# Performance work log

Hardware: AMD Instinct MI355X
Metric: run time of the kernel (lower is better)

The kernel has to match this reference:

```python
import jax, jax.numpy as jnp
import numpy as np

N, E, DIN, H0, H1, HEADS = 50000, 600000, 128, 64, 64, 4
NEG_SLOPE = 0.2
BN_EPS = 1e-5


def setup_inputs() -> dict:
    key = jax.random.key(0)
    ks = iter(jax.random.split(key, 40))
    def p(shape, s=0.05):
        return jax.random.normal(next(ks), shape, jnp.float32) * s
    inp = {}
    inp['x'] = jax.random.normal(next(ks), (N, DIN), jnp.float32)
    inp['edge_index'] = jax.random.randint(next(ks), (2, E), 0, N, dtype=jnp.int32)
    inp['gcn1_w'] = p((DIN, H0)); inp['gcn1_b'] = p((H0,))
    inp['gcn2_w'] = p((H0, H1)); inp['gcn2_b'] = p((H1,))
    inp['gat1_w'] = p((DIN, HEADS * H0))
    inp['gat1_asrc'] = p((HEADS, H0)); inp['gat1_adst'] = p((HEADS, H0))
    inp['gat1_b'] = p((HEADS * H0,))
    inp['gat2_w'] = p((HEADS * H0, H1))
    inp['gat2_asrc'] = p((1, H1)); inp['gat2_adst'] = p((1, H1))
    inp['gat2_b'] = p((H1,))
    inp['sage1_wl'] = p((DIN, H0)); inp['sage1_bl'] = p((H0,)); inp['sage1_wr'] = p((DIN, H0))
    inp['sage2_wl'] = p((H0, H1)); inp['sage2_bl'] = p((H1,)); inp['sage2_wr'] = p((H0, H1))
    inp['bn_gcn_g'] = jnp.ones((H1,), jnp.float32); inp['bn_gcn_b'] = jnp.zeros((H1,), jnp.float32)
    inp['bn_gat_g'] = jnp.ones((H1,), jnp.float32); inp['bn_gat_b'] = jnp.zeros((H1,), jnp.float32)
    inp['bn_sage_g'] = jnp.ones((H1,), jnp.float32); inp['bn_sage_b'] = jnp.zeros((H1,), jnp.float32)
    inp['fc1_w'] = p((3 * H1, H1)); inp['fc1_b'] = p((H1,))
    inp['fc2_w'] = p((H1, 2)); inp['fc2_b'] = p((2,))
    return inp


def _gcn(x, w, b, src, dst, n):
    h = x @ w
    loop = jnp.arange(n)
    s = jnp.concatenate([src, loop]); d = jnp.concatenate([dst, loop])
    deg = jax.ops.segment_sum(jnp.ones(d.shape, h.dtype), d, n)
    dinv = jax.lax.rsqrt(jnp.maximum(deg, 1.0))  # deg >= 1 due to self-loops
    norm = dinv[s] * dinv[d]
    out = jax.ops.segment_sum(h[s] * norm[:, None], d, n)
    return out + b


def _gat(x, w, asrc, adst, b, src, dst, n, heads, outc, concat):
    # GATConv with self-loops; per-destination softmax over incoming edges
    h = (x @ w).reshape(n, heads, outc)
    loop = jnp.arange(n)
    s = jnp.concatenate([src, loop]); d = jnp.concatenate([dst, loop])
    a_s = jnp.einsum('nhc,hc->nh', h, asrc)
    a_d = jnp.einsum('nhc,hc->nh', h, adst)
    e = a_s[s] + a_d[d]                           # [Etot, H]
    e = jnp.where(e > 0, e, NEG_SLOPE * e)        # leaky relu
    emax = jax.ops.segment_max(e, d, n)           # every node has a self-loop
    ex = jnp.exp(e - emax[d])
    denom = jax.ops.segment_sum(ex, d, n)
    alpha = ex / (denom[d] + 1e-16)               # [Etot, H]
    out = jax.ops.segment_sum(h[s] * alpha[:, :, None], d, n)  # [n, H, C]
    out = out.reshape(n, heads * outc) if concat else out.mean(axis=1)
    return out + b


def _sage(x, wl, bl, wr, src, dst, n):
    # SAGEConv (mean aggr): lin_l(mean_j x_j) + lin_r(x_i)
    deg = jax.ops.segment_sum(jnp.ones(src.shape, x.dtype), dst, n)
    agg = jax.ops.segment_sum(x[src], dst, n) / jnp.maximum(deg, 1.0)[:, None]
    return agg @ wl + bl + x @ wr


def _bn(x, g, b):
    m = x.mean(0)
    v = x.var(0)
    return (x - m) * jax.lax.rsqrt(v + BN_EPS) * g + b


def reference(x, edge_index, gcn1_w, gcn1_b, gcn2_w, gcn2_b,
              gat1_w, gat1_asrc, gat1_adst, gat1_b,
              gat2_w, gat2_asrc, gat2_adst, gat2_b,
              sage1_wl, sage1_bl, sage1_wr, sage2_wl, sage2_bl, sage2_wr,
              bn_gcn_g, bn_gcn_b, bn_gat_g, bn_gat_b, bn_sage_g, bn_sage_b,
              fc1_w, fc1_b, fc2_w, fc2_b):
    src, dst = edge_index[0], edge_index[1]
    n = x.shape[0]
    g = jax.nn.relu(_gcn(x, gcn1_w, gcn1_b, src, dst, n))
    g = _bn(jax.nn.relu(_gcn(g, gcn2_w, gcn2_b, src, dst, n)), bn_gcn_g, bn_gcn_b)
    a = jax.nn.elu(_gat(x, gat1_w, gat1_asrc, gat1_adst, gat1_b, src, dst, n, HEADS, H0, True))
    a = _bn(jax.nn.elu(_gat(a, gat2_w, gat2_asrc, gat2_adst, gat2_b, src, dst, n, 1, H1, False)), bn_gat_g, bn_gat_b)
    s = jax.nn.relu(_sage(x, sage1_wl, sage1_bl, sage1_wr, src, dst, n))
    s = _bn(jax.nn.relu(_sage(s, sage2_wl, sage2_bl, sage2_wr, src, dst, n)), bn_sage_g, bn_sage_b)
    out = jnp.concatenate([g, a, s], axis=-1)
    h = jax.nn.relu(out @ fc1_w + fc1_b)
    return h @ fc2_w + fc2_b
```

## Files before the change

kernel.cpp:

```cpp
#include <hip/hip_runtime.h>
#include <math.h>

#define NEG_SLOPE 0.2f
#define BN_EPS 1e-5f

typedef short short8 __attribute__((ext_vector_type(8)));
typedef float floatx16 __attribute__((ext_vector_type(16)));

__device__ __forceinline__ float d_leaky(float x){ return x > 0.f ? x : NEG_SLOPE * x; }
__device__ __forceinline__ float d_elu(float x){ return x > 0.f ? x : expm1f(x); }

__device__ __forceinline__ unsigned short f2bf_rne(float f){
  unsigned int u = __float_as_uint(f);
  unsigned int r = (u + 0x7fffu + ((u >> 16) & 1u)) >> 16;
  return (unsigned short)r;
}
__device__ __forceinline__ float bf2f(unsigned short h){ return __uint_as_float((unsigned int)h << 16); }
__device__ __forceinline__ float2 bf2x(unsigned int u){
  float2 r;
  r.x = __uint_as_float(u << 16);
  r.y = __uint_as_float(u & 0xffff0000u);
  return r;
}

__device__ __forceinline__ float wave_sum(float v){
  #pragma unroll
  for (int off = 32; off > 0; off >>= 1) v += __shfl_xor(v, off, 64);
  return v;
}
__device__ __forceinline__ int wave_scan_incl(int v, int lane){
  #pragma unroll
  for (int off = 1; off < 64; off <<= 1){
    int u = __shfl_up(v, off, 64);
    if (lane >= off) v += u;
  }
  return v;
}

__global__ void k_count(const int* __restrict__ dst, int* __restrict__ deg, int E){
  int e = blockIdx.x * blockDim.x + threadIdx.x;
  if (e < E) atomicAdd(&deg[dst[e]], 1);
}

__global__ __launch_bounds__(256) void k_scan_a(const int* __restrict__ deg, int* __restrict__ bsum, int n){
  int t = threadIdx.x;
  int base = blockIdx.x * 1024 + t * 4;
  int d0=0,d1=0,d2=0,d3=0;
  if (base + 3 < n){ int4 v = *(const int4*)(deg + base); d0=v.x; d1=v.y; d2=v.z; d3=v.w; }
  else {
    if (base   < n) d0 = deg[base];
    if (base+1 < n) d1 = deg[base+1];
    if (base+2 < n) d2 = deg[base+2];
    if (base+3 < n) d3 = deg[base+3];
  }
  int s = d0+d1+d2+d3;
  __shared__ int wsm[4];
  int lane = t & 63, w = t >> 6;
  int incl = wave_scan_incl(s, lane);
  if (lane == 63) wsm[w] = incl;
  __syncthreads();
  if (t == 0) bsum[blockIdx.x] = wsm[0]+wsm[1]+wsm[2]+wsm[3];
}

__global__ void k_scan_b(int* __restrict__ bsum, int* __restrict__ rowp, int nb, int n){
  int t = threadIdx.x;
  int v = (t < nb) ? bsum[t] : 0;
  int incl = wave_scan_incl(v, t);
  if (t < nb) bsum[t] = incl - v;
  if (t == 63) rowp[n] = incl;
}

__global__ __launch_bounds__(256) void k_scan_c(const int* __restrict__ deg, const int* __restrict__ bsum,
                                                int* __restrict__ rowp, float* __restrict__ dinv,
                                                float* __restrict__ sdinv, int n){
  int t = threadIdx.x;
  int base = blockIdx.x * 1024 + t * 4;
  int d0=0,d1=0,d2=0,d3=0;
  if (base + 3 < n){ int4 v = *(const int4*)(deg + base); d0=v.x; d1=v.y; d2=v.z; d3=v.w; }
  else {
    if (base   < n) d0 = deg[base];
    if (base+1 < n) d1 = deg[base+1];
    if (base+2 < n) d2 = deg[base+2];
    if (base+3 < n) d3 = deg[base+3];
  }
  int s = d0+d1+d2+d3;
  __shared__ int wsm[4];
  int lane = t & 63, w = t >> 6;
  int incl = wave_scan_incl(s, lane);
  if (lane == 63) wsm[w] = incl;
  __syncthreads();
  int woff = 0;
  #pragma unroll
  for (int j = 0; j < 4; j++) if (j < w) woff += wsm[j];
  int r = bsum[blockIdx.x] + woff + incl - s;
  int dd[4] = {d0,d1,d2,d3};
  #pragma unroll
  for (int j = 0; j < 4; j++){
    int i = base + j;
    if (i < n){
      rowp[i] = r;
      dinv[i] = rsqrtf((float)(dd[j] + 1));
      sdinv[i] = 1.0f / fmaxf((float)dd[j], 1.0f);
    }
    r += dd[j];
  }
}

__global__ void k_scatter(const int* __restrict__ src, const int* __restrict__ dst,
                          const int* __restrict__ rowp, int* __restrict__ fill,
                          int* __restrict__ colv, int* __restrict__ dstv, int E){
  int e = blockIdx.x * blockDim.x + threadIdx.x;
  if (e < E){
    int d = dst[e];
    int pos = rowp[d] + atomicAdd(&fill[d], 1);
    colv[pos] = src[e];
    dstv[pos] = d;
  }
}

__global__ void k_asplit(const float* __restrict__ a, unsigned short* __restrict__ h,
                         unsigned short* __restrict__ l, int total){
  int i = blockIdx.x * blockDim.x + threadIdx.x;
  if (i < total){
    float v = a[i];
    unsigned short hh = f2bf_rne(v);
    h[i] = hh;
    l[i] = f2bf_rne(v - bf2f(hh));
  }
}

struct WDesc { const float* w; unsigned short* th; unsigned short* tl; int K; int Nc; int perm; };
struct WPack { WDesc d[8]; };
__global__ void k_wsplit(WPack p){
  WDesc w = p.d[blockIdx.y];
  int total = w.K * w.Nc;
  for (int i = blockIdx.x * blockDim.x + threadIdx.x; i < total; i += gridDim.x * blockDim.x){
    int k = i / w.Nc, n = i % w.Nc;
    int kd = (w.perm == 1) ? ((k & 63) * 4 + (k >> 6)) : k;
    int nd = (w.perm == 2) ? (((n & 63) << 2) | (n >> 6)) : n;
    float v = w.w[i];
    unsigned short h = f2bf_rne(v);
    w.th[(size_t)nd * w.K + kd] = h;
    w.tl[(size_t)nd * w.K + kd] = f2bf_rne(v - bf2f(h));
  }
}

__device__ __forceinline__ void gemm_term(floatx16& acc0, floatx16& acc1,
    const unsigned short* __restrict__ Ah, const unsigned short* __restrict__ Al,
    const unsigned short* __restrict__ Bh, const unsigned short* __restrict__ Bl,
    int K, int lda, int arow, int lr, int ko8){
  const unsigned short* ap  = Ah + (size_t)arow * lda + ko8;
  const unsigned short* alp = Al ? Al + (size_t)arow * lda + ko8 : nullptr;
  const unsigned short* bh0 = Bh + (size_t)lr * K + ko8;
  const unsigned short* bl0 = Bl + (size_t)lr * K + ko8;
  const unsigned short* bh1 = bh0 + (size_t)32 * K;
  const unsigned short* bl1 = bl0 + (size_t)32 * K;
  for (int k0 = 0; k0 < K; k0 += 16){
    short8 a  = *(const short8*)(ap + k0);
    short8 h0 = *(const short8*)(bh0 + k0);
    short8 l0 = *(const short8*)(bl0 + k0);
    short8 h1 = *(const short8*)(bh1 + k0);
    short8 l1 = *(const short8*)(bl1 + k0);
    if (alp){
      short8 a2 = *(const short8*)(alp + k0);
      acc0 = __builtin_amdgcn_mfma_f32_32x32x16_bf16(a2, h0, acc0, 0, 0, 0);
      acc1 = __builtin_amdgcn_mfma_f32_32x32x16_bf16(a2, h1, acc1, 0, 0, 0);
    }
    acc0 = __builtin_amdgcn_mfma_f32_32x32x16_bf16(a, l0, acc0, 0, 0, 0);
    acc0 = __builtin_amdgcn_mfma_f32_32x32x16_bf16(a, h0, acc0, 0, 0, 0);
    acc1 = __builtin_amdgcn_mfma_f32_32x32x16_bf16(a, l1, acc1, 0, 0, 0);
    acc1 = __builtin_amdgcn_mfma_f32_32x32x16_bf16(a, h1, acc1, 0, 0, 0);
  }
}

struct BDesc {
  const unsigned short *A1h, *A1l, *B1h, *B1l;
  const unsigned short *A2h, *A2l, *B2h, *B2l;
  int K1, lda1, K2, lda2;
  const float* bias;
  unsigned short* out; int ldc, coloff, act;
};
struct BPack { BDesc d[3]; };
__global__ __launch_bounds__(256) void k_gemm_b(BPack p, int M){
  BDesc d = p.d[blockIdx.y];
  int wave = threadIdx.x >> 6, lane = threadIdx.x & 63;
  int m0 = blockIdx.x * 128 + wave * 32;
  int lr = lane & 31;
  int ko8 = (lane >> 5) * 8;
  floatx16 acc0 = {0,0,0,0,0,0,0,0,0,0,0,0,0,0,0,0};
  floatx16 acc1 = {0,0,0,0,0,0,0,0,0,0,0,0,0,0,0,0};
  int arow = m0 + lr; if (arow >= M) arow = M - 1;
  gemm_term(acc0, acc1, d.A1h, d.A1l, d.B1h, d.B1l, d.K1, d.lda1, arow, lr, ko8);
  if (d.K2) gemm_term(acc0, acc1, d.A2h, d.A2l, d.B2h, d.B2l, d.K2, d.lda2, arow, lr, ko8);
  int col0 = lr, col1 = lr + 32;
  float bias0 = d.bias ? d.bias[col0] : 0.f;
  float bias1 = d.bias ? d.bias[col1] : 0.f;
  int rbase = m0 + 4 * (lane >> 5);
  #pragma unroll
  for (int reg = 0; reg < 16; reg++){
    int row = rbase + (reg & 3) + 8 * (reg >> 2);
    if (row >= M) continue;
    float v0 = acc0[reg] + bias0;
    float v1 = acc1[reg] + bias1;
    if (d.act){ v0 = fmaxf(v0, 0.f); v1 = fmaxf(v1, 0.f); }
    d.out[(size_t)row * d.ldc + d.coloff + col0] = f2bf_rne(v0);
    d.out[(size_t)row * d.ldc + d.coloff + col1] = f2bf_rne(v1);
  }
}

__global__ __launch_bounds__(256) void k_gemm320(
    const unsigned short* __restrict__ Ah, const unsigned short* __restrict__ Al,
    const unsigned short* __restrict__ Bh, const unsigned short* __restrict__ Bl,
    unsigned short* __restrict__ C1, unsigned short* __restrict__ C2, int M)
{
  const int K = 128;
  int wave = threadIdx.x >> 6, lane = threadIdx.x & 63;
  int m0 = blockIdx.x * 128 + wave * 32;
  int n0 = blockIdx.y * 64;
  int lr = lane & 31;
  int ko8 = (lane >> 5) * 8;
  floatx16 acc0 = {0,0,0,0,0,0,0,0,0,0,0,0,0,0,0,0};
  floatx16 acc1 = {0,0,0,0,0,0,0,0,0,0,0,0,0,0,0,0};
  int arow = m0 + lr; if (arow >= M) arow = M - 1;
  const unsigned short* ap_h = Ah + (size_t)arow * K + ko8;
  const unsigned short* ap_l = Al + (size_t)arow * K + ko8;
  const unsigned short* bp_h0 = Bh + (size_t)(n0 + lr) * K + ko8;
  const unsigned short* bp_l0 = Bl + (size_t)(n0 + lr) * K + ko8;
  const unsigned short* bp_h1 = bp_h0 + (size_t)32 * K;
  const unsigned short* bp_l1 = bp_l0 + (size_t)32 * K;
  for (int k0 = 0; k0 < K; k0 += 16){
    short8 a_h  = *(const short8*)(ap_h + k0);
    short8 a_l  = *(const short8*)(ap_l + k0);
    short8 b_h0 = *(const short8*)(bp_h0 + k0);
    short8 b_l0 = *(const short8*)(bp_l0 + k0);
    short8 b_h1 = *(const short8*)(bp_h1 + k0);
    short8 b_l1 = *(const short8*)(bp_l1 + k0);
    acc0 = __builtin_amdgcn_mfma_f32_32x32x16_bf16(a_l, b_h0, acc0, 0, 0, 0);
    acc0 = __builtin_amdgcn_mfma_f32_32x32x16_bf16(a_h, b_l0, acc0, 0, 0, 0);
    acc0 = __builtin_amdgcn_mfma_f32_32x32x16_bf16(a_h, b_h0, acc0, 0, 0, 0);
    acc1 = __builtin_amdgcn_mfma_f32_32x32x16_bf16(a_l, b_h1, acc1, 0, 0, 0);
    acc1 = __builtin_amdgcn_mfma_f32_32x32x16_bf16(a_h, b_l1, acc1, 0, 0, 0);
    acc1 = __builtin_amdgcn_mfma_f32_32x32x16_bf16(a_h, b_h1, acc1, 0, 0, 0);
  }
  int col0 = n0 + lr, col1 = col0 + 32;
  unsigned short* Cp; int ld, c0, c1;
  if (col0 >= 256){ Cp = C2; ld = 64; c0 = col0 - 256; c1 = col1 - 256; }
  else { Cp = C1; ld = 256; c0 = col0; c1 = col1; }
  int rbase = m0 + 4 * (lane >> 5);
  #pragma unroll
  for (int reg = 0; reg < 16; reg++){
    int row = rbase + (reg & 3) + 8 * (reg >> 2);
    if (row >= M) continue;
    Cp[(size_t)row * ld + c0] = f2bf_rne(acc0[reg]);
    Cp[(size_t)row * ld + c1] = f2bf_rne(acc1[reg]);
  }
}

__global__ __launch_bounds__(256) void k_gat_attn4(
    const unsigned short* __restrict__ h, const float* __restrict__ asrc,
    const float* __restrict__ adst, float* __restrict__ a_s, float* __restrict__ a_d, int n){
  int node = blockIdx.x * 4 + (threadIdx.x >> 6);
  int c = threadIdx.x & 63;
  if (node >= n) return;
  uint2 u = *(const uint2*)(h + (size_t)node * 256 + c * 4);
  float2 p0 = bf2x(u.x), p1 = bf2x(u.y);
  float s0 = wave_sum(p0.x * asrc[c]);
  float s1 = wave_sum(p0.y * asrc[64 + c]);
  float s2 = wave_sum(p1.x * asrc[128 + c]);
  float s3 = wave_sum(p1.y * asrc[192 + c]);
  float d0 = wave_sum(p0.x * adst[c]);
  float d1 = wave_sum(p0.y * adst[64 + c]);
  float d2 = wave_sum(p1.x * adst[128 + c]);
  float d3 = wave_sum(p1.y * adst[192 + c]);
  if (c == 0){
    *(float4*)(a_s + (size_t)node * 4) = make_float4(s0, s1, s2, s3);
    *(float4*)(a_d + (size_t)node * 4) = make_float4(d0, d1, d2, d3);
  }
}

__global__ __launch_bounds__(256) void k_gat_attn1(
    const unsigned short* __restrict__ h, int ld, const float* __restrict__ asrc,
    const float* __restrict__ adst, float* __restrict__ a_s, float* __restrict__ a_d, int n){
  int node = blockIdx.x * 4 + (threadIdx.x >> 6);
  int c = threadIdx.x & 63;
  if (node >= n) return;
  float v = bf2f(h[(size_t)node * ld + c]);
  float s = wave_sum(v * asrc[c]);
  float d = wave_sum(v * adst[c]);
  if (c == 0){ a_s[node] = s; a_d[node] = d; }
}

__global__ void k_edge_w4(const int* __restrict__ colv, const int* __restrict__ dstv,
                          const float* __restrict__ a_s, const float* __restrict__ a_d,
                          float* __restrict__ w4, int E){
  int i = blockIdx.x * blockDim.x + threadIdx.x;
  if (i >= E) return;
  float4 s4 = *(const float4*)(a_s + (size_t)colv[i] * 4);
  float4 d4 = *(const float4*)(a_d + (size_t)dstv[i] * 4);
  float4 w;
  w.x = __expf(d_leaky(s4.x + d4.x));
  w.y = __expf(d_leaky(s4.y + d4.y));
  w.z = __expf(d_leaky(s4.z + d4.z));
  w.w = __expf(d_leaky(s4.w + d4.w));
  *(float4*)(w4 + (size_t)i * 4) = w;
}

__global__ void k_edge_w1(const int* __restrict__ colv, const int* __restrict__ dstv,
                          const float* __restrict__ a_s, const float* __restrict__ a_d,
                          float* __restrict__ w1, int E){
  int i = blockIdx.x * blockDim.x + threadIdx.x;
  if (i >= E) return;
  w1[i] = __expf(d_leaky(a_s[colv[i]] + a_d[dstv[i]]));
}

__global__ __launch_bounds__(256) void k_gat_agg4(
    const unsigned short* __restrict__ h, const int* __restrict__ rowp,
    const int* __restrict__ colv, const float* __restrict__ w4,
    const float* __restrict__ a_s, const float* __restrict__ a_d,
    const float* __restrict__ bias, unsigned short* __restrict__ outh, int n){
  int node = blockIdx.x * 4 + (threadIdx.x >> 6);
  int c = threadIdx.x & 63;
  if (node >= n) return;
  float4 asn = *(const float4*)(a_s + (size_t)node * 4);
  float4 adn = *(const float4*)(a_d + (size_t)node * 4);
  float ws0 = __expf(d_leaky(asn.x + adn.x));
  float ws1 = __expf(d_leaky(asn.y + adn.y));
  float ws2 = __expf(d_leaky(asn.z + adn.z));
  float ws3 = __expf(d_leaky(asn.w + adn.w));
  uint2 su = *(const uint2*)(h + (size_t)node * 256 + c * 4);
  float2 sp0 = bf2x(su.x), sp1 = bf2x(su.y);
  float den0 = ws0, den1 = ws1, den2 = ws2, den3 = ws3;
  float acc0 = ws0 * sp0.x, acc1 = ws1 * sp0.y, acc2 = ws2 * sp1.x, acc3 = ws3 * sp1.y;
  int b = rowp[node], e = rowp[node + 1];
  int i = b;
  for (; i + 8 <= e; i += 8){
    int s[8]; float4 w[8]; uint2 hv[8];
    #pragma unroll
    for (int j = 0; j < 8; j++) s[j] = colv[i + j];
    #pragma unroll
    for (int j = 0; j < 8; j++) w[j] = *(const float4*)(w4 + (size_t)(i + j) * 4);
    #pragma unroll
    for (int j = 0; j < 8; j++) hv[j] = *(const uint2*)(h + (size_t)s[j] * 256 + c * 4);
    #pragma unroll
    for (int j = 0; j < 8; j++){
      float2 a = bf2x(hv[j].x), bb = bf2x(hv[j].y);
      den0 += w[j].x; den1 += w[j].y; den2 += w[j].z; den3 += w[j].w;
      acc0 += w[j].x * a.x;  acc1 += w[j].y * a.y;
      acc2 += w[j].z * bb.x; acc3 += w[j].w * bb.y;
    }
  }
  for (; i < e; i++){
    int s = colv[i];
    float4 w = *(const float4*)(w4 + (size_t)i * 4);
    uint2 hv = *(const uint2*)(h + (size_t)s * 256 + c * 4);
    float2 a = bf2x(hv.x), bb = bf2x(hv.y);
    den0 += w.x; den1 += w.y; den2 += w.z; den3 += w.w;
    acc0 += w.x * a.x;  acc1 += w.y * a.y;
    acc2 += w.z * bb.x; acc3 += w.w * bb.y;
  }
  float v0 = d_elu(acc0 / (den0 + 1e-16f) + bias[c]);
  float v1 = d_elu(acc1 / (den1 + 1e-16f) + bias[64 + c]);
  float v2 = d_elu(acc2 / (den2 + 1e-16f) + bias[128 + c]);
  float v3 = d_elu(acc3 / (den3 + 1e-16f) + bias[192 + c]);
  uint2 oh;
  oh.x = (unsigned int)f2bf_rne(v0) | ((unsigned int)f2bf_rne(v1) << 16);
  oh.y = (unsigned int)f2bf_rne(v2) | ((unsigned int)f2bf_rne(v3) << 16);
  *(uint2*)(outh + (size_t)node * 256 + c * 4) = oh;
}

__global__ __launch_bounds__(256) void k_f1(
    const unsigned short* __restrict__ xh,
    const unsigned short* __restrict__ g1h,
    const int* __restrict__ rowp, const int* __restrict__ colv,
    const float* __restrict__ dinv, const float* __restrict__ sdinv,
    const float* __restrict__ gcn1_b,
    unsigned short* __restrict__ aggXh,
    unsigned short* __restrict__ g2h,
    int n){
  int node = blockIdx.x * 4 + (threadIdx.x >> 6);
  int c = threadIdx.x & 63;
  if (node >= n) return;
  float di = dinv[node];
  float gacc = di * bf2f(g1h[(size_t)node * 64 + c]);
  float sx0 = 0.f, sx1 = 0.f;
  int b = rowp[node], e = rowp[node + 1];
  int i = b;
  for (; i + 8 <= e; i += 8){
    int s[8]; float w[8]; unsigned short hg[8]; unsigned int hx[8];
    #pragma unroll
    for (int j = 0; j < 8; j++) s[j] = colv[i + j];
    #pragma unroll
    for (int j = 0; j < 8; j++) w[j] = dinv[s[j]];
    #pragma unroll
    for (int j = 0; j < 8; j++) hg[j] = g1h[(size_t)s[j] * 64 + c];
    #pragma unroll
    for (int j = 0; j < 8; j++) hx[j] = *(const unsigned int*)(xh + (size_t)s[j] * 128 + c * 2);
    #pragma unroll
    for (int j = 0; j < 8; j++){
      gacc += w[j] * bf2f(hg[j]);
      float2 p = bf2x(hx[j]); sx0 += p.x; sx1 += p.y;
    }
  }
  for (; i < e; i++){
    int s = colv[i];
    gacc += dinv[s] * bf2f(g1h[(size_t)s * 64 + c]);
    float2 p = bf2x(*(const unsigned int*)(xh + (size_t)s * 128 + c * 2));
    sx0 += p.x; sx1 += p.y;
  }
  g2h[(size_t)node * 64 + c] = f2bf_rne(fmaxf(di * gacc + gcn1_b[c], 0.f));
  float sd = sdinv[node];
  *(unsigned int*)(aggXh + (size_t)node * 128 + c * 2) =
      (unsigned int)f2bf_rne(sx0 * sd) | ((unsigned int)f2bf_rne(sx1 * sd) << 16);
}

__global__ __launch_bounds__(256) void k_f2(
    const unsigned short* __restrict__ m192,
    const int* __restrict__ rowp, const int* __restrict__ colv,
    const float* __restrict__ w1, const float* __restrict__ a_s, const float* __restrict__ a_d,
    const float* __restrict__ dinv, const float* __restrict__ sdinv,
    const float* __restrict__ gat2_b, const float* __restrict__ gcn2_b,
    unsigned short* __restrict__ cat,
    unsigned short* __restrict__ aggSh,
    int n){
  int node = blockIdx.x * 4 + (threadIdx.x >> 6);
  int c = threadIdx.x & 63;
  if (node >= n) return;
  float di = dinv[node];
  const unsigned short* srow = m192 + (size_t)node * 192;
  float tden = __expf(d_leaky(a_s[node] + a_d[node]));
  float tacc = tden * bf2f(srow[c]);
  float gacc = di * bf2f(srow[64 + c]);
  float sacc = 0.f;
  int b = rowp[node], e = rowp[node + 1];
  int i = b;
  for (; i + 8 <= e; i += 8){
    int s[8]; float w[8]; unsigned short ht[8], hg[8], hs[8];
    #pragma unroll
    for (int j = 0; j < 8; j++) s[j] = colv[i + j];
    #pragma unroll
    for (int j = 0; j < 8; j++) w[j] = w1[i + j];
    #pragma unroll
    for (int j = 0; j < 8; j++){
      const unsigned short* r = m192 + (size_t)s[j] * 192;
      ht[j] = r[c]; hg[j] = r[64 + c]; hs[j] = r[128 + c];
    }
    #pragma unroll
    for (int j = 0; j < 8; j++){
      tden += w[j]; tacc += w[j] * bf2f(ht[j]);
      gacc += dinv[s[j]] * bf2f(hg[j]);
      sacc += bf2f(hs[j]);
    }
  }
  for (; i < e; i++){
    int s = colv[i];
    float w = w1[i];
    const unsigned short* r = m192 + (size_t)s * 192;
    tden += w; tacc += w * bf2f(r[c]);
    gacc += dinv[s] * bf2f(r[64 + c]);
    sacc += bf2f(r[128 + c]);
  }
  cat[(size_t)node * 192 + 64 + c] = f2bf_rne(d_elu(tacc / (tden + 1e-16f) + gat2_b[c]));
  cat[(size_t)node * 192 + c] = f2bf_rne(fmaxf(di * gacc + gcn2_b[c], 0.f));
  aggSh[(size_t)node * 64 + c] = f2bf_rne(sacc * sdinv[node]);
}

__global__ void k_bn_stats3(const unsigned short* __restrict__ x,
                            float* __restrict__ bnGCN, float* __restrict__ bnGAT,
                            float* __restrict__ bnSAGE, int n){
  int seg = blockIdx.y;
  float* sums = (seg == 0) ? bnGCN : (seg == 1) ? bnGAT : bnSAGE;
  int co = seg * 64;
  int c = threadIdx.x & 63;
  int rl = threadIdx.x >> 6;
  float s = 0.f, q = 0.f;
  for (int r = blockIdx.x * 4 + rl; r < n; r += gridDim.x * 4){
    float v = bf2f(x[(size_t)r * 192 + co + c]);
    s += v; q += v * v;
  }
  __shared__ float ls[4][64], lq[4][64];
  ls[rl][c] = s; lq[rl][c] = q;
  __syncthreads();
  if (rl == 0){
    s = ls[0][c] + ls[1][c] + ls[2][c] + ls[3][c];
    q = lq[0][c] + lq[1][c] + lq[2][c] + lq[3][c];
    atomicAdd(&sums[c], s);
    atomicAdd(&sums[64 + c], q);
  }
}

__global__ __launch_bounds__(256) void k_bnfold(
    const float* __restrict__ bnGCN, const float* __restrict__ bnGAT, const float* __restrict__ bnSAGE,
    const float* __restrict__ gg, const float* __restrict__ gb,
    const float* __restrict__ ag, const float* __restrict__ ab,
    const float* __restrict__ sg, const float* __restrict__ sb,
    const float* __restrict__ w, const float* __restrict__ wb, float nf,
    unsigned short* __restrict__ fwh, unsigned short* __restrict__ fwl, float* __restrict__ fb)
{
  int tid = threadIdx.x;
  auto st = [&](int c, float& s, float& t){
    int cc = c & 63;
    const float *bn, *g, *b;
    if (c < 64){ bn = bnGCN; g = gg; b = gb; }
    else if (c < 128){ bn = bnGAT; g = ag; b = ab; }
    else { bn = bnSAGE; g = sg; b = sb; }
    float m = bn[cc] / nf;
    float var = bn[64 + cc] / nf - m * m;
    float inv = rsqrtf(var + BN_EPS);
    s = inv * g[cc];
    t = b[cc] - m * inv * g[cc];
  };
  if (tid < 64){
    float acc = wb[tid];
    for (int c = 0; c < 192; c++){
      float s, t; st(c, s, t);
      acc += t * w[c * 64 + tid];
    }
    fb[tid] = acc;
  }
  for (int i = tid; i < 192 * 64; i += 256){
    int c = i >> 6, nn = i & 63;
    float s, t; st(c, s, t);
    float v = s * w[i];
    unsigned short hh = f2bf_rne(v);
    fwh[nn * 192 + c] = hh;
    fwl[nn * 192 + c] = f2bf_rne(v - bf2f(hh));
  }
}

__global__ void k_fc2(const unsigned short* __restrict__ h, const float* __restrict__ w,
                      const float* __restrict__ b, float* __restrict__ out, int n){
  int node = blockIdx.x * 4 + (threadIdx.x >> 6);
  int lane = threadIdx.x & 63;
  if (node >= n) return;
  float v = bf2f(h[(size_t)node * 64 + lane]);
  float p0 = wave_sum(v * w[lane * 2 + 0]);
  float p1 = wave_sum(v * w[lane * 2 + 1]);
  if (lane == 0){
    out[node * 2 + 0] = p0 + b[0];
    out[node * 2 + 1] = p1 + b[1];
  }
}

extern "C" void kernel_launch(void* const* d_in, const int* in_sizes, int n_in,
                              void* d_out, int out_size, void* d_ws, size_t ws_size,
                              hipStream_t stream){
  (void)n_in; (void)out_size; (void)ws_size;
  const float* x        = (const float*)d_in[0];
  const int*   ei       = (const int*)  d_in[1];
  const float* gcn1_w   = (const float*)d_in[2];
  const float* gcn1_b   = (const float*)d_in[3];
  const float* gcn2_w   = (const float*)d_in[4];
  const float* gcn2_b   = (const float*)d_in[5];
  const float* gat1_w   = (const float*)d_in[6];
  const float* gat1_as  = (const float*)d_in[7];
  const float* gat1_ad  = (const float*)d_in[8];
  const float* gat1_b   = (const float*)d_in[9];
  const float* gat2_w   = (const float*)d_in[10];
  const float* gat2_as  = (const float*)d_in[11];
  const float* gat2_ad  = (const float*)d_in[12];
  const float* gat2_b   = (const float*)d_in[13];
  const float* sage1_wl = (const float*)d_in[14];
  const float* sage1_bl = (const float*)d_in[15];
  const float* sage1_wr = (const float*)d_in[16];
  const float* sage2_wl = (const float*)d_in[17];
  const float* sage2_bl = (const float*)d_in[18];
  const float* sage2_wr = (const float*)d_in[19];
  const float* bn_gcn_g = (const float*)d_in[20];
  const float* bn_gcn_b = (const float*)d_in[21];
  const float* bn_gat_g = (const float*)d_in[22];
  const float* bn_gat_b = (const float*)d_in[23];
  const float* bn_sage_g= (const float*)d_in[24];
  const float* bn_sage_b= (const float*)d_in[25];
  const float* fc1_w    = (const float*)d_in[26];
  const float* fc1_b    = (const float*)d_in[27];
  const float* fc2_w    = (const float*)d_in[28];
  const float* fc2_b    = (const float*)d_in[29];
  float* out = (float*)d_out;

  const int N = in_sizes[0] / 128;
  const int E = in_sizes[1] / 2;
  const int* src = ei;
  const int* dst = ei + E;
  const int nb = (N + 1023) / 1024;

  char* ws = (char*)d_ws;
  size_t off = 0;
  auto alloc = [&](size_t bytes) -> void* {
    void* p = ws + off;
    off = (off + bytes + 255) & ~(size_t)255;
    return p;
  };
  char* zbase = (char*)alloc(0);
  int*   deg   = (int*)  alloc((size_t)N * 4);
  int*   fill  = (int*)  alloc((size_t)N * 4);
  float* bnA   = (float*)alloc(128 * 4);
  float* bnB   = (float*)alloc(128 * 4);
  float* bnC   = (float*)alloc(128 * 4);
  size_t zbytes = (size_t)((char*)alloc(0) - zbase);
  int*   rowp  = (int*)  alloc((size_t)(N + 1) * 4);
  int*   colv  = (int*)  alloc((size_t)E * 4);
  int*   dstv  = (int*)  alloc((size_t)E * 4);
  int*   bsum  = (int*)  alloc(64 * 4);
  float* dinv  = (float*)alloc((size_t)N * 4);
  float* sdinv = (float*)alloc((size_t)N * 4);
  float* as1   = (float*)alloc((size_t)N * 4 * 4);
  float* ad1   = (float*)alloc((size_t)N * 4 * 4);
  float* as2   = (float*)alloc((size_t)N * 4);
  float* ad2   = (float*)alloc((size_t)N * 4);
  float* w4    = (float*)alloc((size_t)E * 4 * 4);
  float* w1    = (float*)alloc((size_t)E * 4);
  unsigned short* xh    = (unsigned short*)alloc((size_t)N * 128 * 2);
  unsigned short* xl    = (unsigned short*)alloc((size_t)N * 128 * 2);
  unsigned short* gath  = (unsigned short*)alloc((size_t)N * 256 * 2);
  unsigned short* oh    = (unsigned short*)alloc((size_t)N * 256 * 2);
  unsigned short* g1h   = (unsigned short*)alloc((size_t)N * 64 * 2);
  unsigned short* g2h   = (unsigned short*)alloc((size_t)N * 64 * 2);
  unsigned short* aggXh = (unsigned short*)alloc((size_t)N * 128 * 2);
  unsigned short* aggSh = (unsigned short*)alloc((size_t)N * 64 * 2);
  unsigned short* m192  = (unsigned short*)alloc((size_t)N * 192 * 2);
  unsigned short* cath  = (unsigned short*)alloc((size_t)N * 192 * 2);
  unsigned short* t1bf  = (unsigned short*)alloc((size_t)N * 64 * 2);
  unsigned short* b320h = (unsigned short*)alloc((size_t)320 * 128 * 2);
  unsigned short* b320l = (unsigned short*)alloc((size_t)320 * 128 * 2);
  unsigned short* gcn2h = (unsigned short*)alloc((size_t)64 * 64 * 2);
  unsigned short* gcn2l = (unsigned short*)alloc((size_t)64 * 64 * 2);
  unsigned short* gat2h = (unsigned short*)alloc((size_t)64 * 256 * 2);
  unsigned short* gat2l = (unsigned short*)alloc((size_t)64 * 256 * 2);
  unsigned short* s1wlh = (unsigned short*)alloc((size_t)64 * 128 * 2);
  unsigned short* s1wll = (unsigned short*)alloc((size_t)64 * 128 * 2);
  unsigned short* s1wrh = (unsigned short*)alloc((size_t)64 * 128 * 2);
  unsigned short* s1wrl = (unsigned short*)alloc((size_t)64 * 128 * 2);
  unsigned short* s2wlh = (unsigned short*)alloc((size_t)64 * 64 * 2);
  unsigned short* s2wll = (unsigned short*)alloc((size_t)64 * 64 * 2);
  unsigned short* s2wrh = (unsigned short*)alloc((size_t)64 * 64 * 2);
  unsigned short* s2wrl = (unsigned short*)alloc((size_t)64 * 64 * 2);
  unsigned short* fwh   = (unsigned short*)alloc((size_t)64 * 192 * 2);
  unsigned short* fwl   = (unsigned short*)alloc((size_t)64 * 192 * 2);
  float* fb             = (float*)alloc(64 * 4);

  hipMemsetAsync(zbase, 0, zbytes, stream);

  k_count <<<(E + 255) / 256, 256, 0, stream>>>(dst, deg, E);
  k_scan_a<<<nb, 256, 0, stream>>>(deg, bsum, N);
  k_scan_b<<<1, 64, 0, stream>>>(bsum, rowp, nb, N);
  k_scan_c<<<nb, 256, 0, stream>>>(deg, bsum, rowp, dinv, sdinv, N);
  k_scatter<<<(E + 255) / 256, 256, 0, stream>>>(src, dst, rowp, fill, colv, dstv, E);

  {
    WPack p;
    p.d[0] = {gat1_w, b320h, b320l, 128, 256, 2};
    p.d[1] = {gcn1_w, b320h + 256 * 128, b320l + 256 * 128, 128, 64, 0};
    p.d[2] = {gat2_w, gat2h, gat2l, 256, 64, 1};
    p.d[3] = {sage1_wl, s1wlh, s1wll, 128, 64, 0};
    p.d[4] = {sage1_wr, s1wrh, s1wrl, 128, 64, 0};
    p.d[5] = {sage2_wl, s2wlh, s2wll, 64, 64, 0};
    p.d[6] = {sage2_wr, s2wrh, s2wrl, 64, 64, 0};
    p.d[7] = {gcn2_w, gcn2h, gcn2l, 64, 64, 0};
    dim3 g(32, 8);
    k_wsplit<<<g, 256, 0, stream>>>(p);
  }
  k_asplit<<<(N * 128 + 255) / 256, 256, 0, stream>>>(x, xh, xl, N * 128);

  const int gx = (N + 127) / 128;
  const int gn = (N + 3) / 4;

  {
    dim3 g(gx, 5);
    k_gemm320<<<g, 256, 0, stream>>>(xh, xl, b320h, b320l, gath, g1h, N);
  }
  k_gat_attn4<<<gn, 256, 0, stream>>>(gath, gat1_as, gat1_ad, as1, ad1, N);
  k_edge_w4<<<(E + 255) / 256, 256, 0, stream>>>(colv, dstv, as1, ad1, w4, E);
  k_f1<<<gn, 256, 0, stream>>>(xh, g1h, rowp, colv, dinv, sdinv, gcn1_b, aggXh, g2h, N);
  k_gat_agg4<<<gn, 256, 0, stream>>>(gath, rowp, colv, w4, as1, ad1, gat1_b, oh, N);

  {
    BPack p;
    p.d[0] = {oh, nullptr, gat2h, gat2l, nullptr, nullptr, nullptr, nullptr,
              256, 256, 0, 0, nullptr, m192, 192, 0, 0};
    p.d[1] = {g2h, nullptr, gcn2h, gcn2l, nullptr, nullptr, nullptr, nullptr,
              64, 64, 0, 0, nullptr, m192, 192, 64, 0};
    p.d[2] = {aggXh, nullptr, s1wlh, s1wll, xh, xl, s1wrh, s1wrl,
              128, 128, 128, 128, sage1_bl, m192, 192, 128, 1};
    dim3 g(gx, 3);
    k_gemm_b<<<g, 256, 0, stream>>>(p, N);
  }
  k_gat_attn1<<<gn, 256, 0, stream>>>(m192, 192, gat2_as, gat2_ad, as2, ad2, N);
  k_edge_w1<<<(E + 255) / 256, 256, 0, stream>>>(colv, dstv, as2, ad2, w1, E);
  k_f2<<<gn, 256, 0, stream>>>(m192, rowp, colv, w1, as2, ad2, dinv, sdinv,
                               gat2_b, gcn2_b, cath, aggSh, N);

  {
    BPack p;
    p.d[0] = {aggSh, nullptr, s2wlh, s2wll, m192 + 128, nullptr, s2wrh, s2wrl,
              64, 64, 64, 192, sage2_bl, cath, 192, 128, 1};
    p.d[1] = p.d[0]; p.d[2] = p.d[0];
    dim3 g(gx, 1);
    k_gemm_b<<<g, 256, 0, stream>>>(p, N);
  }

  {
    dim3 g(128, 3);
    k_bn_stats3<<<g, 256, 0, stream>>>(cath, bnB, bnA, bnC, N);
  }
  k_bnfold<<<1, 256, 0, stream>>>(bnB, bnA, bnC,
                                  bn_gcn_g, bn_gcn_b, bn_gat_g, bn_gat_b, bn_sage_g, bn_sage_b,
                                  fc1_w, fc1_b, (float)N, fwh, fwl, fb);

  {
    BPack p;
    p.d[0] = {cath, nullptr, fwh, fwl, nullptr, nullptr, nullptr, nullptr,
              192, 192, 0, 0, fb, t1bf, 64, 0, 1};
    p.d[1] = p.d[0]; p.d[2] = p.d[0];
    dim3 g(gx, 1);
    k_gemm_b<<<g, 256, 0, stream>>>(p, N);
  }
  k_fc2<<<gn, 256, 0, stream>>>(t1bf, fc2_w, fc2_b, out, N);
}
```

Measured before the change: 656.3 us.

## Fuse layer-1 GAT/GCN/SAGE aggregations, store bf16 edge weights, fold fc2 into gemm

```diff
diff --git a/kernel.cpp b/kernel.cpp
--- a/kernel.cpp
+++ b/kernel.cpp
@@ -179,6 +179,7 @@
   int K1, lda1, K2, lda2;
   const float* bias;
   unsigned short* out; int ldc, coloff, act;
+  const float* fc2w; const float* fc2b; float* outf;
 };
 struct BPack { BDesc d[3]; };
 __global__ __launch_bounds__(256) void k_gemm_b(BPack p, int M){
@@ -195,16 +196,35 @@
   int col0 = lr, col1 = lr + 32;
   float bias0 = d.bias ? d.bias[col0] : 0.f;
   float bias1 = d.bias ? d.bias[col1] : 0.f;
+  float w00 = 0.f, w01 = 0.f, w10 = 0.f, w11 = 0.f;
+  if (d.fc2w){
+    w00 = d.fc2w[col0 * 2 + 0]; w01 = d.fc2w[col0 * 2 + 1];
+    w10 = d.fc2w[col1 * 2 + 0]; w11 = d.fc2w[col1 * 2 + 1];
+  }
   int rbase = m0 + 4 * (lane >> 5);
   #pragma unroll
   for (int reg = 0; reg < 16; reg++){
     int row = rbase + (reg & 3) + 8 * (reg >> 2);
-    if (row >= M) continue;
     float v0 = acc0[reg] + bias0;
     float v1 = acc1[reg] + bias1;
     if (d.act){ v0 = fmaxf(v0, 0.f); v1 = fmaxf(v1, 0.f); }
-    d.out[(size_t)row * d.ldc + d.coloff + col0] = f2bf_rne(v0);
-    d.out[(size_t)row * d.ldc + d.coloff + col1] = f2bf_rne(v1);
+    if (d.out && row < M){
+      d.out[(size_t)row * d.ldc + d.coloff + col0] = f2bf_rne(v0);
+      d.out[(size_t)row * d.ldc + d.coloff + col1] = f2bf_rne(v1);
+    }
+    if (d.fc2w){
+      float p0 = v0 * w00 + v1 * w10;
+      float p1 = v0 * w01 + v1 * w11;
+      #pragma unroll
+      for (int off = 16; off > 0; off >>= 1){
+        p0 += __shfl_xor(p0, off, 64);
+        p1 += __shfl_xor(p1, off, 64);
+      }
+      if ((lane & 31) == 0 && row < M){
+        d.outf[(size_t)row * 2 + 0] = p0 + d.fc2b[0];
+        d.outf[(size_t)row * 2 + 1] = p1 + d.fc2b[1];
+      }
+    }
   }
 }
 
@@ -292,17 +312,19 @@
 
 __global__ void k_edge_w4(const int* __restrict__ colv, const int* __restrict__ dstv,
                           const float* __restrict__ a_s, const float* __restrict__ a_d,
-                          float* __restrict__ w4, int E){
+                          unsigned short* __restrict__ w4b, int E){
   int i = blockIdx.x * blockDim.x + threadIdx.x;
   if (i >= E) return;
   float4 s4 = *(const float4*)(a_s + (size_t)colv[i] * 4);
   float4 d4 = *(const float4*)(a_d + (size_t)dstv[i] * 4);
-  float4 w;
-  w.x = __expf(d_leaky(s4.x + d4.x));
-  w.y = __expf(d_leaky(s4.y + d4.y));
-  w.z = __expf(d_leaky(s4.z + d4.z));
-  w.w = __expf(d_leaky(s4.w + d4.w));
-  *(float4*)(w4 + (size_t)i * 4) = w;
+  float w0 = __expf(d_leaky(s4.x + d4.x));
+  float w1 = __expf(d_leaky(s4.y + d4.y));
+  float w2 = __expf(d_leaky(s4.z + d4.z));
+  float w3 = __expf(d_leaky(s4.w + d4.w));
+  uint2 q;
+  q.x = (unsigned int)f2bf_rne(w0) | ((unsigned int)f2bf_rne(w1) << 16);
+  q.y = (unsigned int)f2bf_rne(w2) | ((unsigned int)f2bf_rne(w3) << 16);
+  *(uint2*)(w4b + (size_t)i * 4) = q;
 }
 
 __global__ void k_edge_w1(const int* __restrict__ colv, const int* __restrict__ dstv,
@@ -313,11 +335,17 @@
   w1[i] = __expf(d_leaky(a_s[colv[i]] + a_d[dstv[i]]));
 }
 
-__global__ __launch_bounds__(256) void k_gat_agg4(
-    const unsigned short* __restrict__ h, const int* __restrict__ rowp,
-    const int* __restrict__ colv, const float* __restrict__ w4,
+__global__ __launch_bounds__(256) void k_l1agg(
+    const unsigned short* __restrict__ gath, const unsigned short* __restrict__ xh,
+    const unsigned short* __restrict__ g1h,
+    const int* __restrict__ rowp, const int* __restrict__ colv,
+    const unsigned short* __restrict__ w4b,
     const float* __restrict__ a_s, const float* __restrict__ a_d,
-    const float* __restrict__ bias, unsigned short* __restrict__ outh, int n){
+    const float* __restrict__ gat1_b, const float* __restrict__ gcn1_b,
+    const float* __restrict__ dinv, const float* __restrict__ sdinv,
+    unsigned short* __restrict__ oh, unsigned short* __restrict__ g2h,
+    unsigned short* __restrict__ aggXh, int n)
+{
   int node = blockIdx.x * 4 + (threadIdx.x >> 6);
   int c = threadIdx.x & 63;
   if (node >= n) return;
@@ -327,86 +355,61 @@
   float ws1 = __expf(d_leaky(asn.y + adn.y));
   float ws2 = __expf(d_leaky(asn.z + adn.z));
   float ws3 = __expf(d_leaky(asn.w + adn.w));
-  uint2 su = *(const uint2*)(h + (size_t)node * 256 + c * 4);
+  uint2 su = *(const uint2*)(gath + (size_t)node * 256 + c * 4);
   float2 sp0 = bf2x(su.x), sp1 = bf2x(su.y);
   float den0 = ws0, den1 = ws1, den2 = ws2, den3 = ws3;
   float acc0 = ws0 * sp0.x, acc1 = ws1 * sp0.y, acc2 = ws2 * sp1.x, acc3 = ws3 * sp1.y;
-  int b = rowp[node], e = rowp[node + 1];
-  int i = b;
-  for (; i + 8 <= e; i += 8){
-    int s[8]; float4 w[8]; uint2 hv[8];
-    #pragma unroll
-    for (int j = 0; j < 8; j++) s[j] = colv[i + j];
-    #pragma unroll
-    for (int j = 0; j < 8; j++) w[j] = *(const float4*)(w4 + (size_t)(i + j) * 4);
-    #pragma unroll
-    for (int j = 0; j < 8; j++) hv[j] = *(const uint2*)(h + (size_t)s[j] * 256 + c * 4);
-    #pragma unroll
-    for (int j = 0; j < 8; j++){
-      float2 a = bf2x(hv[j].x), bb = bf2x(hv[j].y);
-      den0 += w[j].x; den1 += w[j].y; den2 += w[j].z; den3 += w[j].w;
-      acc0 += w[j].x * a.x;  acc1 += w[j].y * a.y;
-      acc2 += w[j].z * bb.x; acc3 += w[j].w * bb.y;
-    }
-  }
-  for (; i < e; i++){
-    int s = colv[i];
-    float4 w = *(const float4*)(w4 + (size_t)i * 4);
-    uint2 hv = *(const uint2*)(h + (size_t)s * 256 + c * 4);
-    float2 a = bf2x(hv.x), bb = bf2x(hv.y);
-    den0 += w.x; den1 += w.y; den2 += w.z; den3 += w.w;
-    acc0 += w.x * a.x;  acc1 += w.y * a.y;
-    acc2 += w.z * bb.x; acc3 += w.w * bb.y;
-  }
-  float v0 = d_elu(acc0 / (den0 + 1e-16f) + bias[c]);
-  float v1 = d_elu(acc1 / (den1 + 1e-16f) + bias[64 + c]);
-  float v2 = d_elu(acc2 / (den2 + 1e-16f) + bias[128 + c]);
-  float v3 = d_elu(acc3 / (den3 + 1e-16f) + bias[192 + c]);
-  uint2 oh;
-  oh.x = (unsigned int)f2bf_rne(v0) | ((unsigned int)f2bf_rne(v1) << 16);
-  oh.y = (unsigned int)f2bf_rne(v2) | ((unsigned int)f2bf_rne(v3) << 16);
-  *(uint2*)(outh + (size_t)node * 256 + c * 4) = oh;
-}
-
-__global__ __launch_bounds__(256) void k_f1(
-    const unsigned short* __restrict__ xh,
-    const unsigned short* __restrict__ g1h,
-    const int* __restrict__ rowp, const int* __restrict__ colv,
-    const float* __restrict__ dinv, const float* __restrict__ sdinv,
-    const float* __restrict__ gcn1_b,
-    unsigned short* __restrict__ aggXh,
-    unsigned short* __restrict__ g2h,
-    int n){
-  int node = blockIdx.x * 4 + (threadIdx.x >> 6);
-  int c = threadIdx.x & 63;
-  if (node >= n) return;
   float di = dinv[node];
   float gacc = di * bf2f(g1h[(size_t)node * 64 + c]);
   float sx0 = 0.f, sx1 = 0.f;
   int b = rowp[node], e = rowp[node + 1];
-  int i = b;
-  for (; i + 8 <= e; i += 8){
-    int s[8]; float w[8]; unsigned short hg[8]; unsigned int hx[8];
-    #pragma unroll
-    for (int j = 0; j < 8; j++) s[j] = colv[i + j];
-    #pragma unroll
-    for (int j = 0; j < 8; j++) w[j] = dinv[s[j]];
+  for (int i = b; i < e; i += 8){
+    int idx[8]; float mm[8]; int s[8];
+    #pragma unroll
+    for (int j = 0; j < 8; j++){
+      int t = i + j;
+      mm[j] = (t < e) ? 1.f : 0.f;
+      idx[j] = (t < e) ? t : (e - 1);
+    }
+    #pragma unroll
+    for (int j = 0; j < 8; j++) s[j] = colv[idx[j]];
+    uint2 wq[8];
+    #pragma unroll
+    for (int j = 0; j < 8; j++) wq[j] = *(const uint2*)(w4b + (size_t)idx[j] * 4);
+    uint2 hv[8];
+    #pragma unroll
+    for (int j = 0; j < 8; j++) hv[j] = *(const uint2*)(gath + (size_t)s[j] * 256 + c * 4);
+    unsigned int hx[8];
+    #pragma unroll
+    for (int j = 0; j < 8; j++) hx[j] = *(const unsigned int*)(xh + (size_t)s[j] * 128 + c * 2);
+    unsigned short hg[8];
     #pragma unroll
     for (int j = 0; j < 8; j++) hg[j] = g1h[(size_t)s[j] * 64 + c];
-    #pragma unroll
-    for (int j = 0; j < 8; j++) hx[j] = *(const unsigned int*)(xh + (size_t)s[j] * 128 + c * 2);
+    float wd[8];
+    #pragma unroll
+    for (int j = 0; j < 8; j++) wd[j] = dinv[s[j]];
     #pragma unroll
     for (int j = 0; j < 8; j++){
-      gacc += w[j] * bf2f(hg[j]);
-      float2 p = bf2x(hx[j]); sx0 += p.x; sx1 += p.y;
-    }
-  }
-  for (; i < e; i++){
-    int s = colv[i];
-    gacc += dinv[s] * bf2f(g1h[(size_t)s * 64 + c]);
-    float2 p = bf2x(*(const unsigned int*)(xh + (size_t)s * 128 + c * 2));
-    sx0 += p.x; sx1 += p.y;
-  }
+      float m = mm[j];
+      float2 w01 = bf2x(wq[j].x), w23 = bf2x(wq[j].y);
+      float w0 = m * w01.x, w1 = m * w01.y, w2 = m * w23.x, w3 = m * w23.y;
+      float2 a = bf2x(hv[j].x), bb = bf2x(hv[j].y);
+      den0 += w0; den1 += w1; den2 += w2; den3 += w3;
+      acc0 += w0 * a.x;  acc1 += w1 * a.y;
+      acc2 += w2 * bb.x; acc3 += w3 * bb.y;
+      gacc += m * wd[j] * bf2f(hg[j]);
+      float2 p = bf2x(hx[j]);
+      sx0 += m * p.x; sx1 += m * p.y;
+    }
+  }
+  float v0 = d_elu(acc0 / (den0 + 1e-16f) + gat1_b[c]);
+  float v1 = d_elu(acc1 / (den1 + 1e-16f) + gat1_b[64 + c]);
+  float v2 = d_elu(acc2 / (den2 + 1e-16f) + gat1_b[128 + c]);
+  float v3 = d_elu(acc3 / (den3 + 1e-16f) + gat1_b[192 + c]);
+  uint2 ohv;
+  ohv.x = (unsigned int)f2bf_rne(v0) | ((unsigned int)f2bf_rne(v1) << 16);
+  ohv.y = (unsigned int)f2bf_rne(v2) | ((unsigned int)f2bf_rne(v3) << 16);
+  *(uint2*)(oh + (size_t)node * 256 + c * 4) = ohv;
   g2h[(size_t)node * 64 + c] = f2bf_rne(fmaxf(di * gacc + gcn1_b[c], 0.f));
   float sd = sdinv[node];
   *(unsigned int*)(aggXh + (size_t)node * 128 + c * 2) =
@@ -432,32 +435,34 @@
   float gacc = di * bf2f(srow[64 + c]);
   float sacc = 0.f;
   int b = rowp[node], e = rowp[node + 1];
-  int i = b;
-  for (; i + 8 <= e; i += 8){
-    int s[8]; float w[8]; unsigned short ht[8], hg[8], hs[8];
-    #pragma unroll
-    for (int j = 0; j < 8; j++) s[j] = colv[i + j];
-    #pragma unroll
-    for (int j = 0; j < 8; j++) w[j] = w1[i + j];
+  for (int i = b; i < e; i += 8){
+    int idx[8]; float mm[8]; int s[8];
+    #pragma unroll
+    for (int j = 0; j < 8; j++){
+      int t = i + j;
+      mm[j] = (t < e) ? 1.f : 0.f;
+      idx[j] = (t < e) ? t : (e - 1);
+    }
+    #pragma unroll
+    for (int j = 0; j < 8; j++) s[j] = colv[idx[j]];
+    float w[8];
+    #pragma unroll
+    for (int j = 0; j < 8; j++) w[j] = w1[idx[j]] * mm[j];
+    unsigned short ht[8], hg[8], hs[8];
     #pragma unroll
     for (int j = 0; j < 8; j++){
       const unsigned short* r = m192 + (size_t)s[j] * 192;
       ht[j] = r[c]; hg[j] = r[64 + c]; hs[j] = r[128 + c];
     }
+    float wd[8];
+    #pragma unroll
+    for (int j = 0; j < 8; j++) wd[j] = dinv[s[j]];
     #pragma unroll
     for (int j = 0; j < 8; j++){
       tden += w[j]; tacc += w[j] * bf2f(ht[j]);
-      gacc += dinv[s[j]] * bf2f(hg[j]);
-      sacc += bf2f(hs[j]);
-    }
-  }
-  for (; i < e; i++){
-    int s = colv[i];
-    float w = w1[i];
-    const unsigned short* r = m192 + (size_t)s * 192;
-    tden += w; tacc += w * bf2f(r[c]);
-    gacc += dinv[s] * bf2f(r[64 + c]);
-    sacc += bf2f(r[128 + c]);
+      gacc += mm[j] * wd[j] * bf2f(hg[j]);
+      sacc += mm[j] * bf2f(hs[j]);
+    }
   }
   cat[(size_t)node * 192 + 64 + c] = f2bf_rne(d_elu(tacc / (tden + 1e-16f) + gat2_b[c]));
   cat[(size_t)node * 192 + c] = f2bf_rne(fmaxf(di * gacc + gcn2_b[c], 0.f));
@@ -524,20 +529,6 @@
     unsigned short hh = f2bf_rne(v);
     fwh[nn * 192 + c] = hh;
     fwl[nn * 192 + c] = f2bf_rne(v - bf2f(hh));
-  }
-}
-
-__global__ void k_fc2(const unsigned short* __restrict__ h, const float* __restrict__ w,
-                      const float* __restrict__ b, float* __restrict__ out, int n){
-  int node = blockIdx.x * 4 + (threadIdx.x >> 6);
-  int lane = threadIdx.x & 63;
-  if (node >= n) return;
-  float v = bf2f(h[(size_t)node * 64 + lane]);
-  float p0 = wave_sum(v * w[lane * 2 + 0]);
-  float p1 = wave_sum(v * w[lane * 2 + 1]);
-  if (lane == 0){
-    out[node * 2 + 0] = p0 + b[0];
-    out[node * 2 + 1] = p1 + b[1];
   }
 }
 
@@ -607,7 +598,7 @@
   float* ad1   = (float*)alloc((size_t)N * 4 * 4);
   float* as2   = (float*)alloc((size_t)N * 4);
   float* ad2   = (float*)alloc((size_t)N * 4);
-  float* w4    = (float*)alloc((size_t)E * 4 * 4);
+  unsigned short* w4b = (unsigned short*)alloc((size_t)E * 4 * 2);
   float* w1    = (float*)alloc((size_t)E * 4);
   unsigned short* xh    = (unsigned short*)alloc((size_t)N * 128 * 2);
   unsigned short* xl    = (unsigned short*)alloc((size_t)N * 128 * 2);
@@ -619,7 +610,6 @@
   unsigned short* aggSh = (unsigned short*)alloc((size_t)N * 64 * 2);
   unsigned short* m192  = (unsigned short*)alloc((size_t)N * 192 * 2);
   unsigned short* cath  = (unsigned short*)alloc((size_t)N * 192 * 2);
-  unsigned short* t1bf  = (unsigned short*)alloc((size_t)N * 64 * 2);
   unsigned short* b320h = (unsigned short*)alloc((size_t)320 * 128 * 2);
   unsigned short* b320l = (unsigned short*)alloc((size_t)320 * 128 * 2);
   unsigned short* gcn2h = (unsigned short*)alloc((size_t)64 * 64 * 2);
@@ -669,18 +659,18 @@
     k_gemm320<<<g, 256, 0, stream>>>(xh, xl, b320h, b320l, gath, g1h, N);
   }
   k_gat_attn4<<<gn, 256, 0, stream>>>(gath, gat1_as, gat1_ad, as1, ad1, N);
-  k_edge_w4<<<(E + 255) / 256, 256, 0, stream>>>(colv, dstv, as1, ad1, w4, E);
-  k_f1<<<gn, 256, 0, stream>>>(xh, g1h, rowp, colv, dinv, sdinv, gcn1_b, aggXh, g2h, N);
-  k_gat_agg4<<<gn, 256, 0, stream>>>(gath, rowp, colv, w4, as1, ad1, gat1_b, oh, N);
+  k_edge_w4<<<(E + 255) / 256, 256, 0, stream>>>(colv, dstv, as1, ad1, w4b, E);
+  k_l1agg<<<gn, 256, 0, stream>>>(gath, xh, g1h, rowp, colv, w4b, as1, ad1,
+                                  gat1_b, gcn1_b, dinv, sdinv, oh, g2h, aggXh, N);
 
   {
     BPack p;
     p.d[0] = {oh, nullptr, gat2h, gat2l, nullptr, nullptr, nullptr, nullptr,
-              256, 256, 0, 0, nullptr, m192, 192, 0, 0};
+              256, 256, 0, 0, nullptr, m192, 192, 0, 0, nullptr, nullptr, nullptr};
     p.d[1] = {g2h, nullptr, gcn2h, gcn2l, nullptr, nullptr, nullptr, nullptr,
-              64, 64, 0, 0, nullptr, m192, 192, 64, 0};
+              64, 64, 0, 0, nullptr, m192, 192, 64, 0, nullptr, nullptr, nullptr};
     p.d[2] = {aggXh, nullptr, s1wlh, s1wll, xh, xl, s1wrh, s1wrl,
-              128, 128, 128, 128, sage1_bl, m192, 192, 128, 1};
+              128, 128, 128, 128, sage1_bl, m192, 192, 128, 1, nullptr, nullptr, nullptr};
     dim3 g(gx, 3);
     k_gemm_b<<<g, 256, 0, stream>>>(p, N);
   }
@@ -692,7 +682,7 @@
   {
     BPack p;
     p.d[0] = {aggSh, nullptr, s2wlh, s2wll, m192 + 128, nullptr, s2wrh, s2wrl,
-              64, 64, 64, 192, sage2_bl, cath, 192, 128, 1};
+              64, 64, 64, 192, sage2_bl, cath, 192, 128, 1, nullptr, nullptr, nullptr};
     p.d[1] = p.d[0]; p.d[2] = p.d[0];
     dim3 g(gx, 1);
     k_gemm_b<<<g, 256, 0, stream>>>(p, N);
@@ -709,10 +699,9 @@
   {
     BPack p;
     p.d[0] = {cath, nullptr, fwh, fwl, nullptr, nullptr, nullptr, nullptr,
-              192, 192, 0, 0, fb, t1bf, 64, 0, 1};
+              192, 192, 0, 0, fb, nullptr, 64, 0, 1, fc2_w, fc2_b, out};
     p.d[1] = p.d[0]; p.d[2] = p.d[0];
     dim3 g(gx, 1);
     k_gemm_b<<<g, 256, 0, stream>>>(p, N);
   }
-  k_fc2<<<gn, 256, 0, stream>>>(t1bf, fc2_w, fc2_b, out, N);
-}
+}
```

Result: faster. 633.3 us (-3.5%).
